# Kernel tuning notes

Measured on AMD Instinct MI355X. Metric: run time of the kernel, lower is better.

## Reference

```python
import jax, jax.numpy as jnp
import numpy as np

BLOCK_SIZE = 256

def setup_inputs() -> dict:
    key = jax.random.key(0)
    k1, k2, k3 = jax.random.split(key, 3)
    B, H, S, D = 2, 16, 2048, 128
    return {
        "query": jax.random.normal(k1, (B, H, S, D), dtype=jnp.float32),
        "key": jax.random.normal(k2, (B, H, S, D), dtype=jnp.float32),
        "value": jax.random.normal(k3, (B, H, S, D), dtype=jnp.float32),
    }

def reference(query, key, value):
    # Faithful translation of the (non-flash) blocked attention:
    # for each query block i and key block j, a FULL softmax is taken over
    # just that key block, and the per-block outputs are summed over j.
    B, H, S, D = query.shape
    bs = min(BLOCK_SIZE, S)
    nb = S // bs  # S chosen to be a multiple of block_size
    scale = D ** -0.5
    q = query.reshape(B, H, nb, bs, D)
    k = key.reshape(B, H, nb, bs, D)
    v = value.reshape(B, H, nb, bs, D)
    # scores: [B,H,nb_q,nb_k,bs_q,bs_k]
    scores = jnp.einsum('bhiqd,bhjkd->bhijqk', q, k) * scale
    # per key-block softmax (over last axis only, NOT global online softmax)
    w = jax.nn.softmax(scores, axis=-1)
    # weighted values, summed over key blocks j (matches output += block_output)
    out = jnp.einsum('bhijqk,bhjkd->bhiqd', w, v)
    return out.reshape(B, H, S, D)
```

## Files before the change

kernel.cpp:

```cpp
#include <hip/hip_runtime.h>
#include <stdint.h>

#define S_LEN 2048
#define D_DIM 128

typedef __attribute__((ext_vector_type(8)))  short bf16x8;
typedef __attribute__((ext_vector_type(4)))  short bf16x4;
typedef __attribute__((ext_vector_type(4)))  float f32x4;
typedef __attribute__((ext_vector_type(2)))  float f32x2;
typedef __attribute__((ext_vector_type(16))) float f32x16;

__device__ __forceinline__ short f2bf(float f) {
  union { float f; uint32_t u; } c; c.f = f;
  uint32_t u = c.u;
  u += 0x7fffu + ((u >> 16) & 1u);
  return (short)(u >> 16);
}
__device__ __forceinline__ uint32_t pk2bf(float a, float b) {
#if __has_builtin(__builtin_amdgcn_cvt_pk_bf16_f32)
  typedef __attribute__((ext_vector_type(2))) __bf16 bf2;
  union { bf2 v; uint32_t u; } cv;
  cv.v = __builtin_amdgcn_cvt_pk_bf16_f32(a, b);
  return cv.u;
#else
  return (uint32_t)(uint16_t)f2bf(a) | (((uint32_t)(uint16_t)f2bf(b)) << 16);
#endif
}
__device__ __forceinline__ float fexp2(float x) {
#if __has_builtin(__builtin_amdgcn_exp2f)
  return __builtin_amdgcn_exp2f(x);
#else
  return exp2f(x);
#endif
}
__device__ __forceinline__ bf16x8 mk8(uint32_t a, uint32_t b, uint32_t c, uint32_t d) {
  union { uint32_t u[4]; bf16x8 v; } x;
  x.u[0] = a; x.u[1] = b; x.u[2] = c; x.u[3] = d;
  return x.v;
}
__device__ __forceinline__ void gl_lds16(const short* g, short* l) {
  __builtin_amdgcn_global_load_lds((const __attribute__((address_space(1))) void*)g,
                                   (__attribute__((address_space(3))) void*)l, 16, 0, 0);
}

__global__ __launch_bounds__(256) void pre_kernel(
    const float* __restrict__ K, const float* __restrict__ V,
    short* __restrict__ Kb, short* __restrict__ Vt) {
  const int t = threadIdx.x;
  if (blockIdx.x >= 512) {
    int i0 = (blockIdx.x - 512) * 256 + t;
#pragma unroll
    for (int r = 0; r < 4; ++r) {
      int i = i0 + r * 524288;
      f32x4 v = ((const f32x4*)K)[i];
      *(uint2*)(Kb + (size_t)i * 4) = make_uint2(pk2bf(v[0], v[1]), pk2bf(v[2], v[3]));
    }
    return;
  }
  __shared__ __align__(16) uint32_t sU[128][64];
  const int vb = blockIdx.x;
  const int bh = vb >> 4;
  const int k0 = (vb & 15) * 128;
  const float* src = V + ((size_t)bh * S_LEN + k0) * D_DIM;
  {
    const int a = t & 31;
    const int E = 2 * (a & 15);
    const float* s0 = src + (size_t)(t >> 5) * 2 * D_DIM + a * 4;
#pragma unroll
    for (int p = 0; p < 8; ++p) {
      f32x4 vA = *(const f32x4*)(s0 + p * 16 * D_DIM);
      f32x4 vB = *(const f32x4*)(s0 + p * 16 * D_DIM + D_DIM);
      const int k2 = p * 8 + (t >> 5);
      const int col = k2 ^ E;
#pragma unroll
      for (int j = 0; j < 4; ++j)
        sU[4 * a + j][col] = pk2bf(vA[j], vB[j]);
    }
  }
  __syncthreads();
  {
    const int d = t >> 1;
    const int E = 2 * ((t >> 3) & 15);
    short* out = Vt + ((size_t)bh * D_DIM + d) * S_LEN + k0 + (t & 1) * 8;
#pragma unroll
    for (int g = 0; g < 8; ++g) {
      const int pb = g * 16 + (t & 1) * 8;
      const int kb1 = ((pb >> 4) << 4) + ((pb & 15) ? 4 : 0);
      const int k2a = kb1 >> 1;
      const int k2b = k2a + 4;
      uint2 lo = *(const uint2*)&sU[d][k2a ^ E];
      uint2 hi = *(const uint2*)&sU[d][k2b ^ E];
      uint4 o; o.x = lo.x; o.y = lo.y; o.z = hi.x; o.w = hi.y;
      *(uint4*)(out + g * 16) = o;
    }
  }
}

__global__ __launch_bounds__(256, 2) void attn_main(
    const short* __restrict__ Kb, const short* __restrict__ Vt,
    const float* __restrict__ Q, float* __restrict__ O) {
  __shared__ __align__(16) short ring[2][16384];
  __shared__ __align__(16) short sP[4096];
  __shared__ float sRed[128];
  __shared__ float sLinv[64];

  const int t = threadIdx.x;
  const int w = t >> 6;
  const int lane = t & 63;
  const int l31 = lane & 31;
  const int hi = lane >> 5;
  const int h = w & 1;
  const int qp = w >> 1;

  const int b = blockIdx.x;
  const int bh = (b & 7) * 4 + ((b >> 3) & 3);
  const int q0 = (b >> 5) * 64;

  const short* Kh = Kb + (size_t)bh * S_LEN * D_DIM;
  const short* Vh = Vt + (size_t)bh * D_DIM * S_LEN;

  const int kKey = t >> 4;
  const int kG   = (t & 15) ^ (kKey & 15);
  const int vD   = t >> 3;
  const int vG   = (t & 7) ^ (vD & 7);

  auto stageK = [&](int key0, int slot) {
    const short* src = Kh + (size_t)(key0 + kKey) * D_DIM + kG * 8;
    short* dst = &ring[slot][t * 8];
#pragma unroll
    for (int r = 0; r < 4; ++r) gl_lds16(src + r * 16 * D_DIM, dst + r * 2048);
  };
  auto stageV = [&](int key0, int slot) {
    const short* src = Vh + (size_t)vD * S_LEN + key0 + vG * 8;
    short* dst = &ring[slot][8192 + t * 8];
#pragma unroll
    for (int r = 0; r < 4; ++r) gl_lds16(src + (size_t)r * 32 * S_LEN, dst + r * 2048);
  };

  bf16x8 qf[8];
  {
    const float QSCALE = 0.12751743f;
    const float* Qg = Q + ((size_t)bh * S_LEN + q0 + qp * 32 + l31) * D_DIM;
#pragma unroll
    for (int ks = 0; ks < 8; ++ks) {
      f32x4 a = *(const f32x4*)(Qg + ks * 16 + hi * 8);
      f32x4 c = *(const f32x4*)(Qg + ks * 16 + hi * 8 + 4);
      qf[ks] = mk8(pk2bf(a[0] * QSCALE, a[1] * QSCALE), pk2bf(a[2] * QSCALE, a[3] * QSCALE),
                   pk2bf(c[0] * QSCALE, c[1] * QSCALE), pk2bf(c[2] * QSCALE, c[3] * QSCALE));
    }
  }

  int aK[8];
#pragma unroll
  for (int ks = 0; ks < 8; ++ks)
    aK[ks] = (h * 32 + l31) * 128 + (((2 * ks + hi) ^ (l31 & 15)) << 3);
  int aV[4];
#pragma unroll
  for (int u = 0; u < 4; ++u)
    aV[u] = (h * 64 + l31) * 64 + (((u * 2 + hi) ^ (l31 & 7)) << 3);

  f32x16 oa[2], oj[2], ojb[2];
#pragma unroll
  for (int d = 0; d < 2; ++d)
#pragma unroll
    for (int r = 0; r < 16; ++r) { oa[d][r] = 0.f; oj[d][r] = 0.f; ojb[d][r] = 0.f; }

  float ssum = 0.f;
  const int spOwn = ((qp * 2 + h) * 2) * 512 + lane * 8;

  stageK(0, 0); stageV(0, 0);

  for (int j = 0; j < 8; ++j) {
#pragma unroll
    for (int c = 0; c < 4; ++c) {
      const int G = j * 4 + c;
      const int slot = G & 1;
      __syncthreads();
      if (G + 1 < 32) { stageK((G + 1) * 64, slot ^ 1); stageV((G + 1) * 64, slot ^ 1); }

      if (c == 0 && j > 0) {
        f32x4 lv[4];
#pragma unroll
        for (int g = 0; g < 4; ++g) lv[g] = *(const f32x4*)&sLinv[qp * 32 + g * 8 + hi * 4];
#pragma unroll
        for (int d = 0; d < 2; ++d)
#pragma unroll
          for (int r = 0; r < 16; ++r) {
            oa[d][r] += (oj[d][r] + ojb[d][r]) * lv[r >> 2][r & 3];
            oj[d][r] = 0.f;
            ojb[d][r] = 0.f;
          }
      }

      const short* pK = &ring[slot][0];
      f32x16 sc0, sc1;
#pragma unroll
      for (int r = 0; r < 16; ++r) { sc0[r] = 0.f; sc1[r] = 0.f; }
#pragma unroll
      for (int ks = 0; ks < 4; ++ks) {
        bf16x8 a0 = *(const bf16x8*)(pK + aK[2 * ks]);
        bf16x8 a1 = *(const bf16x8*)(pK + aK[2 * ks + 1]);
        sc0 = __builtin_amdgcn_mfma_f32_32x32x16_bf16(a0, qf[2 * ks], sc0, 0, 0, 0);
        sc1 = __builtin_amdgcn_mfma_f32_32x32x16_bf16(a1, qf[2 * ks + 1], sc1, 0, 0, 0);
      }
      f32x16 sc;
#pragma unroll
      for (int r = 0; r < 16; ++r) sc[r] = fexp2(sc0[r] + sc1[r]);

      bf16x8 pf[2];
#pragma unroll
      for (int t2 = 0; t2 < 2; ++t2) {
        pf[t2] = mk8(pk2bf(sc[8 * t2 + 0], sc[8 * t2 + 1]), pk2bf(sc[8 * t2 + 2], sc[8 * t2 + 3]),
                     pk2bf(sc[8 * t2 + 4], sc[8 * t2 + 5]), pk2bf(sc[8 * t2 + 6], sc[8 * t2 + 7]));
        *(bf16x8*)(sP + spOwn + t2 * 512) = pf[t2];
      }
      {
        float a0 = sc[0] + sc[1], a1 = sc[2] + sc[3], a2 = sc[4] + sc[5], a3 = sc[6] + sc[7];
        float a4 = sc[8] + sc[9], a5 = sc[10] + sc[11], a6 = sc[12] + sc[13], a7 = sc[14] + sc[15];
        float b0 = a0 + a1, b1 = a2 + a3, b2 = a4 + a5, b3 = a6 + a7;
        ssum += (b0 + b1) + (b2 + b3);
      }
      if (c == 3) {
        ssum += __shfl_xor(ssum, 32);
        if (lane < 32) sRed[(qp * 32 + l31) * 2 + h] = ssum;
        ssum = 0.f;
      }
      __syncthreads();
      if (c == 3 && h == 0 && lane < 32) {
        f32x2 s2 = *(const f32x2*)&sRed[(qp * 32 + l31) * 2];
        sLinv[qp * 32 + l31] = __fdividef(1.0f, s2[0] + s2[1]);
      }

      const short* pV = &ring[slot][8192];
#pragma unroll
      for (int hw = 0; hw < 2; ++hw)
#pragma unroll
        for (int t2 = 0; t2 < 2; ++t2) {
          bf16x8 a = (hw == h) ? pf[t2]
                               : *(const bf16x8*)(sP + ((qp * 2 + hw) * 2 + t2) * 512 + lane * 8);
#pragma unroll
          for (int dt = 0; dt < 2; ++dt) {
            bf16x8 bv = *(const bf16x8*)(pV + aV[hw * 2 + t2] + dt * 2048);
            if (hw == 0)
              oj[dt] = __builtin_amdgcn_mfma_f32_32x32x16_bf16(a, bv, oj[dt], 0, 0, 0);
            else
              ojb[dt] = __builtin_amdgcn_mfma_f32_32x32x16_bf16(a, bv, ojb[dt], 0, 0, 0);
          }
        }
    }
  }

  __syncthreads();
  {
    f32x4 lv[4];
#pragma unroll
    for (int g = 0; g < 4; ++g) lv[g] = *(const f32x4*)&sLinv[qp * 32 + g * 8 + hi * 4];
    float* Og = O + ((size_t)bh * S_LEN + q0) * D_DIM;
#pragma unroll
    for (int d = 0; d < 2; ++d)
#pragma unroll
      for (int r = 0; r < 16; ++r) {
        float val = oa[d][r] + (oj[d][r] + ojb[d][r]) * lv[r >> 2][r & 3];
        int row = qp * 32 + (r & 3) + 8 * (r >> 2) + 4 * hi;
        int col = h * 64 + d * 32 + l31;
        Og[row * D_DIM + col] = val;
      }
  }
}

extern "C" void kernel_launch(void* const* d_in, const int* in_sizes, int n_in,
                              void* d_out, int out_size, void* d_ws, size_t ws_size,
                              hipStream_t stream) {
  const float* Q = (const float*)d_in[0];
  const float* K = (const float*)d_in[1];
  const float* V = (const float*)d_in[2];
  float* Out = (float*)d_out;
  const size_t tElems = (size_t)32 * S_LEN * D_DIM;

  short* Kb  = (short*)d_ws;
  short* Vtb = Kb + tElems;

  pre_kernel<<<2560, 256, 0, stream>>>(K, V, Kb, Vtb);
  attn_main<<<1024, 256, 0, stream>>>(Kb, Vtb, Q, Out);
}
```

Before: 222.9 us.

## Pre-swizzle V into MFMA fragment layout and load V directly to registers

The V transpose pre-pass now writes V in a fragment-major layout so each lane can load its MFMA B operands straight from global memory into registers, with no LDS staging. The V half of the LDS ring is removed, which halves the ring and LDS footprint and may allow more resident blocks. The per-row reciprocal sum is computed on the fly from sRed instead of through a separate sLinv pass, and the second block barrier becomes a raw waitcnt plus s_barrier. In exchange, V global-load latency now sits directly in each iteration, prefetched only at the start of the same step rather than a step ahead, and every wave re-reads V from global/L2.

```diff
diff --git a/kernel.cpp b/kernel.cpp
--- a/kernel.cpp
+++ b/kernel.cpp
@@ -81,7 +81,8 @@
   {
     const int d = t >> 1;
     const int E = 2 * ((t >> 3) & 15);
-    short* out = Vt + ((size_t)bh * D_DIM + d) * S_LEN + k0 + (t & 1) * 8;
+    short* outB = Vt + (size_t)bh * 262144 + d * 8;
+    const int g0 = k0 >> 3;
 #pragma unroll
     for (int g = 0; g < 8; ++g) {
       const int pb = g * 16 + (t & 1) * 8;
@@ -89,9 +90,9 @@
       const int k2a = kb1 >> 1;
       const int k2b = k2a + 4;
       uint2 lo = *(const uint2*)&sU[d][k2a ^ E];
-      uint2 hi = *(const uint2*)&sU[d][k2b ^ E];
-      uint4 o; o.x = lo.x; o.y = lo.y; o.z = hi.x; o.w = hi.y;
-      *(uint4*)(out + g * 16) = o;
+      uint2 hi2 = *(const uint2*)&sU[d][k2b ^ E];
+      uint4 o; o.x = lo.x; o.y = lo.y; o.z = hi2.x; o.w = hi2.y;
+      *(uint4*)(outB + (size_t)(g0 + (pb >> 3)) * 1024) = o;
     }
   }
 }
@@ -99,10 +100,9 @@
 __global__ __launch_bounds__(256, 2) void attn_main(
     const short* __restrict__ Kb, const short* __restrict__ Vt,
     const float* __restrict__ Q, float* __restrict__ O) {
-  __shared__ __align__(16) short ring[2][16384];
+  __shared__ __align__(16) short ring[2][8192];
   __shared__ __align__(16) short sP[4096];
   __shared__ float sRed[128];
-  __shared__ float sLinv[64];
 
   const int t = threadIdx.x;
   const int w = t >> 6;
@@ -117,12 +117,10 @@
   const int q0 = (b >> 5) * 64;
 
   const short* Kh = Kb + (size_t)bh * S_LEN * D_DIM;
-  const short* Vh = Vt + (size_t)bh * D_DIM * S_LEN;
+  const short* Vh2 = Vt + (size_t)bh * 262144;
 
   const int kKey = t >> 4;
   const int kG   = (t & 15) ^ (kKey & 15);
-  const int vD   = t >> 3;
-  const int vG   = (t & 7) ^ (vD & 7);
 
   auto stageK = [&](int key0, int slot) {
     const short* src = Kh + (size_t)(key0 + kKey) * D_DIM + kG * 8;
@@ -130,12 +128,8 @@
 #pragma unroll
     for (int r = 0; r < 4; ++r) gl_lds16(src + r * 16 * D_DIM, dst + r * 2048);
   };
-  auto stageV = [&](int key0, int slot) {
-    const short* src = Vh + (size_t)vD * S_LEN + key0 + vG * 8;
-    short* dst = &ring[slot][8192 + t * 8];
-#pragma unroll
-    for (int r = 0; r < 4; ++r) gl_lds16(src + (size_t)r * 32 * S_LEN, dst + r * 2048);
-  };
+
+  const short* Vbase = Vh2 + hi * 1024 + (h * 64 + l31) * 8;
 
   bf16x8 qf[8];
   {
@@ -154,10 +148,6 @@
 #pragma unroll
   for (int ks = 0; ks < 8; ++ks)
     aK[ks] = (h * 32 + l31) * 128 + (((2 * ks + hi) ^ (l31 & 15)) << 3);
-  int aV[4];
-#pragma unroll
-  for (int u = 0; u < 4; ++u)
-    aV[u] = (h * 64 + l31) * 64 + (((u * 2 + hi) ^ (l31 & 7)) << 3);
 
   f32x16 oa[2], oj[2], ojb[2];
 #pragma unroll
@@ -168,7 +158,19 @@
   float ssum = 0.f;
   const int spOwn = ((qp * 2 + h) * 2) * 512 + lane * 8;
 
-  stageK(0, 0); stageV(0, 0);
+  auto loadLv = [&](f32x4* lv) {
+#pragma unroll
+    for (int g = 0; g < 4; ++g) {
+      f32x4 p0 = *(const f32x4*)&sRed[(qp * 32 + g * 8 + 4 * hi) * 2];
+      f32x4 p1 = *(const f32x4*)&sRed[(qp * 32 + g * 8 + 4 * hi) * 2 + 4];
+      lv[g][0] = __fdividef(1.0f, p0[0] + p0[1]);
+      lv[g][1] = __fdividef(1.0f, p0[2] + p0[3]);
+      lv[g][2] = __fdividef(1.0f, p1[0] + p1[1]);
+      lv[g][3] = __fdividef(1.0f, p1[2] + p1[3]);
+    }
+  };
+
+  stageK(0, 0);
 
   for (int j = 0; j < 8; ++j) {
 #pragma unroll
@@ -176,12 +178,19 @@
       const int G = j * 4 + c;
       const int slot = G & 1;
       __syncthreads();
-      if (G + 1 < 32) { stageK((G + 1) * 64, slot ^ 1); stageV((G + 1) * 64, slot ^ 1); }
+
+      bf16x8 vf[8];
+#pragma unroll
+      for (int u = 0; u < 4; ++u)
+#pragma unroll
+        for (int dt = 0; dt < 2; ++dt)
+          vf[u * 2 + dt] = *(const bf16x8*)(Vbase + (size_t)G * 8192 + u * 2048 + dt * 256);
+
+      if (G + 1 < 32) stageK((G + 1) * 64, slot ^ 1);
 
       if (c == 0 && j > 0) {
         f32x4 lv[4];
-#pragma unroll
-        for (int g = 0; g < 4; ++g) lv[g] = *(const f32x4*)&sLinv[qp * 32 + g * 8 + hi * 4];
+        loadLv(lv);
 #pragma unroll
         for (int d = 0; d < 2; ++d)
 #pragma unroll
@@ -225,13 +234,9 @@
         if (lane < 32) sRed[(qp * 32 + l31) * 2 + h] = ssum;
         ssum = 0.f;
       }
-      __syncthreads();
-      if (c == 3 && h == 0 && lane < 32) {
-        f32x2 s2 = *(const f32x2*)&sRed[(qp * 32 + l31) * 2];
-        sLinv[qp * 32 + l31] = __fdividef(1.0f, s2[0] + s2[1]);
-      }
-
-      const short* pV = &ring[slot][8192];
+
+      asm volatile("s_waitcnt lgkmcnt(0)\n\ts_barrier" ::: "memory");
+
 #pragma unroll
       for (int hw = 0; hw < 2; ++hw)
 #pragma unroll
@@ -240,7 +245,7 @@
                                : *(const bf16x8*)(sP + ((qp * 2 + hw) * 2 + t2) * 512 + lane * 8);
 #pragma unroll
           for (int dt = 0; dt < 2; ++dt) {
-            bf16x8 bv = *(const bf16x8*)(pV + aV[hw * 2 + t2] + dt * 2048);
+            bf16x8 bv = vf[(hw * 2 + t2) * 2 + dt];
             if (hw == 0)
               oj[dt] = __builtin_amdgcn_mfma_f32_32x32x16_bf16(a, bv, oj[dt], 0, 0, 0);
             else
@@ -253,8 +258,7 @@
   __syncthreads();
   {
     f32x4 lv[4];
-#pragma unroll
-    for (int g = 0; g < 4; ++g) lv[g] = *(const f32x4*)&sLinv[qp * 32 + g * 8 + hi * 4];
+    loadLv(lv);
     float* Og = O + ((size_t)bh * S_LEN + q0) * D_DIM;
 #pragma unroll
     for (int d = 0; d < 2; ++d)
```

Result: slower. 263.5 us (+18.2%).

## Recompute full key-tile scores per wave to drop P exchange and mid-iteration barrier

Applied to the files above, without the earlier changes.

Each wave pair previously split the 64 keys of a tile, exchanged bf16 probabilities through shared memory and needed a second __syncthreads per tile plus a reciprocal stage. Now each wave computes QK^T for all 64 keys redundantly (splitting D for the PV product instead), keeping P in registers, removing the sP buffer and the extra barrier, and computing reciprocals at use. This doubles the QK MFMA and exp work per wave in exchange for fewer barriers and LDS traffic. The sRed write at c==3 and its later read rely on the next iteration's top barrier for ordering.

```diff
diff --git a/kernel.cpp b/kernel.cpp
--- a/kernel.cpp
+++ b/kernel.cpp
@@ -100,16 +100,14 @@
     const short* __restrict__ Kb, const short* __restrict__ Vt,
     const float* __restrict__ Q, float* __restrict__ O) {
   __shared__ __align__(16) short ring[2][16384];
-  __shared__ __align__(16) short sP[4096];
-  __shared__ float sRed[128];
-  __shared__ float sLinv[64];
+  __shared__ float sRed[64];
 
   const int t = threadIdx.x;
   const int w = t >> 6;
   const int lane = t & 63;
   const int l31 = lane & 31;
   const int hi = lane >> 5;
-  const int h = w & 1;
+  const int dh = w & 1;
   const int qp = w >> 1;
 
   const int b = blockIdx.x;
@@ -153,11 +151,11 @@
   int aK[8];
 #pragma unroll
   for (int ks = 0; ks < 8; ++ks)
-    aK[ks] = (h * 32 + l31) * 128 + (((2 * ks + hi) ^ (l31 & 15)) << 3);
+    aK[ks] = l31 * 128 + (((2 * ks + hi) ^ (l31 & 15)) << 3);
   int aV[4];
 #pragma unroll
   for (int u = 0; u < 4; ++u)
-    aV[u] = (h * 64 + l31) * 64 + (((u * 2 + hi) ^ (l31 & 7)) << 3);
+    aV[u] = (dh * 64 + l31) * 64 + (((u * 2 + hi) ^ (l31 & 7)) << 3);
 
   f32x16 oa[2], oj[2], ojb[2];
 #pragma unroll
@@ -166,7 +164,17 @@
     for (int r = 0; r < 16; ++r) { oa[d][r] = 0.f; oj[d][r] = 0.f; ojb[d][r] = 0.f; }
 
   float ssum = 0.f;
-  const int spOwn = ((qp * 2 + h) * 2) * 512 + lane * 8;
+
+  auto loadLv = [&](f32x4* lv) {
+#pragma unroll
+    for (int g = 0; g < 4; ++g) {
+      f32x4 s = *(const f32x4*)&sRed[qp * 32 + g * 8 + 4 * hi];
+      lv[g][0] = __fdividef(1.0f, s[0]);
+      lv[g][1] = __fdividef(1.0f, s[1]);
+      lv[g][2] = __fdividef(1.0f, s[2]);
+      lv[g][3] = __fdividef(1.0f, s[3]);
+    }
+  };
 
   stageK(0, 0); stageV(0, 0);
 
@@ -180,8 +188,7 @@
 
       if (c == 0 && j > 0) {
         f32x4 lv[4];
-#pragma unroll
-        for (int g = 0; g < 4; ++g) lv[g] = *(const f32x4*)&sLinv[qp * 32 + g * 8 + hi * 4];
+        loadLv(lv);
 #pragma unroll
         for (int d = 0; d < 2; ++d)
 #pragma unroll
@@ -197,64 +204,58 @@
 #pragma unroll
       for (int r = 0; r < 16; ++r) { sc0[r] = 0.f; sc1[r] = 0.f; }
 #pragma unroll
-      for (int ks = 0; ks < 4; ++ks) {
-        bf16x8 a0 = *(const bf16x8*)(pK + aK[2 * ks]);
-        bf16x8 a1 = *(const bf16x8*)(pK + aK[2 * ks + 1]);
-        sc0 = __builtin_amdgcn_mfma_f32_32x32x16_bf16(a0, qf[2 * ks], sc0, 0, 0, 0);
-        sc1 = __builtin_amdgcn_mfma_f32_32x32x16_bf16(a1, qf[2 * ks + 1], sc1, 0, 0, 0);
-      }
-      f32x16 sc;
-#pragma unroll
-      for (int r = 0; r < 16; ++r) sc[r] = fexp2(sc0[r] + sc1[r]);
-
-      bf16x8 pf[2];
+      for (int ks = 0; ks < 8; ++ks) {
+        bf16x8 a0 = *(const bf16x8*)(pK + aK[ks]);
+        bf16x8 a1 = *(const bf16x8*)(pK + aK[ks] + 4096);
+        sc0 = __builtin_amdgcn_mfma_f32_32x32x16_bf16(a0, qf[ks], sc0, 0, 0, 0);
+        sc1 = __builtin_amdgcn_mfma_f32_32x32x16_bf16(a1, qf[ks], sc1, 0, 0, 0);
+      }
+#pragma unroll
+      for (int r = 0; r < 16; ++r) { sc0[r] = fexp2(sc0[r]); sc1[r] = fexp2(sc1[r]); }
+
+      bf16x8 pf[4];
 #pragma unroll
       for (int t2 = 0; t2 < 2; ++t2) {
-        pf[t2] = mk8(pk2bf(sc[8 * t2 + 0], sc[8 * t2 + 1]), pk2bf(sc[8 * t2 + 2], sc[8 * t2 + 3]),
-                     pk2bf(sc[8 * t2 + 4], sc[8 * t2 + 5]), pk2bf(sc[8 * t2 + 6], sc[8 * t2 + 7]));
-        *(bf16x8*)(sP + spOwn + t2 * 512) = pf[t2];
+        pf[t2] = mk8(pk2bf(sc0[8 * t2 + 0], sc0[8 * t2 + 1]), pk2bf(sc0[8 * t2 + 2], sc0[8 * t2 + 3]),
+                     pk2bf(sc0[8 * t2 + 4], sc0[8 * t2 + 5]), pk2bf(sc0[8 * t2 + 6], sc0[8 * t2 + 7]));
+        pf[2 + t2] = mk8(pk2bf(sc1[8 * t2 + 0], sc1[8 * t2 + 1]), pk2bf(sc1[8 * t2 + 2], sc1[8 * t2 + 3]),
+                         pk2bf(sc1[8 * t2 + 4], sc1[8 * t2 + 5]), pk2bf(sc1[8 * t2 + 6], sc1[8 * t2 + 7]));
       }
       {
-        float a0 = sc[0] + sc[1], a1 = sc[2] + sc[3], a2 = sc[4] + sc[5], a3 = sc[6] + sc[7];
-        float a4 = sc[8] + sc[9], a5 = sc[10] + sc[11], a6 = sc[12] + sc[13], a7 = sc[14] + sc[15];
-        float b0 = a0 + a1, b1 = a2 + a3, b2 = a4 + a5, b3 = a6 + a7;
-        ssum += (b0 + b1) + (b2 + b3);
+        float a0 = sc0[0] + sc0[1], a1 = sc0[2] + sc0[3], a2 = sc0[4] + sc0[5], a3 = sc0[6] + sc0[7];
+        float a4 = sc0[8] + sc0[9], a5 = sc0[10] + sc0[11], a6 = sc0[12] + sc0[13], a7 = sc0[14] + sc0[15];
+        float b0 = sc1[0] + sc1[1], b1 = sc1[2] + sc1[3], b2 = sc1[4] + sc1[5], b3 = sc1[6] + sc1[7];
+        float b4 = sc1[8] + sc1[9], b5 = sc1[10] + sc1[11], b6 = sc1[12] + sc1[13], b7 = sc1[14] + sc1[15];
+        float c0 = (a0 + a1) + (a2 + a3), c1 = (a4 + a5) + (a6 + a7);
+        float c2 = (b0 + b1) + (b2 + b3), c3 = (b4 + b5) + (b6 + b7);
+        ssum += (c0 + c1) + (c2 + c3);
       }
       if (c == 3) {
         ssum += __shfl_xor(ssum, 32);
-        if (lane < 32) sRed[(qp * 32 + l31) * 2 + h] = ssum;
+        if (dh == 0 && lane < 32) sRed[qp * 32 + l31] = ssum;
         ssum = 0.f;
       }
-      __syncthreads();
-      if (c == 3 && h == 0 && lane < 32) {
-        f32x2 s2 = *(const f32x2*)&sRed[(qp * 32 + l31) * 2];
-        sLinv[qp * 32 + l31] = __fdividef(1.0f, s2[0] + s2[1]);
-      }
 
       const short* pV = &ring[slot][8192];
 #pragma unroll
-      for (int hw = 0; hw < 2; ++hw)
-#pragma unroll
-        for (int t2 = 0; t2 < 2; ++t2) {
-          bf16x8 a = (hw == h) ? pf[t2]
-                               : *(const bf16x8*)(sP + ((qp * 2 + hw) * 2 + t2) * 512 + lane * 8);
-#pragma unroll
-          for (int dt = 0; dt < 2; ++dt) {
-            bf16x8 bv = *(const bf16x8*)(pV + aV[hw * 2 + t2] + dt * 2048);
-            if (hw == 0)
-              oj[dt] = __builtin_amdgcn_mfma_f32_32x32x16_bf16(a, bv, oj[dt], 0, 0, 0);
-            else
-              ojb[dt] = __builtin_amdgcn_mfma_f32_32x32x16_bf16(a, bv, ojb[dt], 0, 0, 0);
-          }
+      for (int u = 0; u < 4; ++u) {
+        bf16x8 a = pf[u];
+#pragma unroll
+        for (int dt = 0; dt < 2; ++dt) {
+          bf16x8 bv = *(const bf16x8*)(pV + aV[u] + dt * 2048);
+          if (u < 2)
+            oj[dt] = __builtin_amdgcn_mfma_f32_32x32x16_bf16(a, bv, oj[dt], 0, 0, 0);
+          else
+            ojb[dt] = __builtin_amdgcn_mfma_f32_32x32x16_bf16(a, bv, ojb[dt], 0, 0, 0);
         }
+      }
     }
   }
 
   __syncthreads();
   {
     f32x4 lv[4];
-#pragma unroll
-    for (int g = 0; g < 4; ++g) lv[g] = *(const f32x4*)&sLinv[qp * 32 + g * 8 + hi * 4];
+    loadLv(lv);
     float* Og = O + ((size_t)bh * S_LEN + q0) * D_DIM;
 #pragma unroll
     for (int d = 0; d < 2; ++d)
@@ -262,7 +263,7 @@
       for (int r = 0; r < 16; ++r) {
         float val = oa[d][r] + (oj[d][r] + ojb[d][r]) * lv[r >> 2][r & 3];
         int row = qp * 32 + (r & 3) + 8 * (r >> 2) + 4 * hi;
-        int col = h * 64 + d * 32 + l31;
+        int col = dh * 64 + d * 32 + l31;
         Og[row * D_DIM + col] = val;
       }
   }
```

New measurement: 312.6 us. +40.2%, slower.

## Software-pipeline PV matmul one chunk behind QK and drop the second barrier

Applied to the files above, without the earlier changes.

Restructures the main loop so that the P·V MFMAs for chunk G-1 run after the QK^T and exp of chunk G. This removes the mid-iteration __syncthreads that separated writing P to shared memory from reading the partner wave's P. V staging is shifted one chunk later, the per-row reciprocal is computed directly from sRed instead of a separate sLinv pass, and a drain step after the loop handles the last PV. The intent is one barrier per chunk instead of two and better overlap of exp/convert work with MFMA, at the cost of more live registers (two P buffers) and trickier slot and rescale timing.

```diff
diff --git a/kernel.cpp b/kernel.cpp
--- a/kernel.cpp
+++ b/kernel.cpp
@@ -102,7 +102,6 @@
   __shared__ __align__(16) short ring[2][16384];
   __shared__ __align__(16) short sP[4096];
   __shared__ float sRed[128];
-  __shared__ float sLinv[64];
 
   const int t = threadIdx.x;
   const int w = t >> 6;
@@ -167,21 +166,44 @@
 
   float ssum = 0.f;
   const int spOwn = ((qp * 2 + h) * 2) * 512 + lane * 8;
-
-  stageK(0, 0); stageV(0, 0);
+  const int spFor = ((qp * 2 + (1 - h)) * 2) * 512 + lane * 8;
+
+  auto loadLv = [&](f32x4* lv) {
+#pragma unroll
+    for (int g = 0; g < 4; ++g) {
+      f32x4 p0 = *(const f32x4*)&sRed[(qp * 32 + g * 8 + 4 * hi) * 2];
+      f32x4 p1 = *(const f32x4*)&sRed[(qp * 32 + g * 8 + 4 * hi) * 2 + 4];
+      lv[g][0] = __fdividef(1.0f, p0[0] + p0[1]);
+      lv[g][1] = __fdividef(1.0f, p0[2] + p0[3]);
+      lv[g][2] = __fdividef(1.0f, p1[0] + p1[1]);
+      lv[g][3] = __fdividef(1.0f, p1[2] + p1[3]);
+    }
+  };
+
+  bf16x8 pfA[2], pfB[2];
+
+  stageK(0, 0);
 
   for (int j = 0; j < 8; ++j) {
 #pragma unroll
     for (int c = 0; c < 4; ++c) {
       const int G = j * 4 + c;
-      const int slot = G & 1;
+      const int kslot = c & 1;
       __syncthreads();
-      if (G + 1 < 32) { stageK((G + 1) * 64, slot ^ 1); stageV((G + 1) * 64, slot ^ 1); }
-
-      if (c == 0 && j > 0) {
+
+      if (G + 1 < 32) stageK((G + 1) * 64, kslot ^ 1);
+      stageV(G * 64, kslot);
+
+      bf16x8 pfF0, pfF1;
+      if (j > 0 || c > 0) {
+        pfF0 = *(const bf16x8*)(sP + spFor);
+        pfF1 = *(const bf16x8*)(sP + spFor + 512);
+      }
+      asm volatile("s_waitcnt lgkmcnt(0)\n\ts_barrier" ::: "memory");
+
+      if (c == 1 && j > 0) {
         f32x4 lv[4];
-#pragma unroll
-        for (int g = 0; g < 4; ++g) lv[g] = *(const f32x4*)&sLinv[qp * 32 + g * 8 + hi * 4];
+        loadLv(lv);
 #pragma unroll
         for (int d = 0; d < 2; ++d)
 #pragma unroll
@@ -192,7 +214,7 @@
           }
       }
 
-      const short* pK = &ring[slot][0];
+      const short* pK = &ring[kslot][0];
       f32x16 sc0, sc1;
 #pragma unroll
       for (int r = 0; r < 16; ++r) { sc0[r] = 0.f; sc1[r] = 0.f; }
@@ -203,20 +225,22 @@
         sc0 = __builtin_amdgcn_mfma_f32_32x32x16_bf16(a0, qf[2 * ks], sc0, 0, 0, 0);
         sc1 = __builtin_amdgcn_mfma_f32_32x32x16_bf16(a1, qf[2 * ks + 1], sc1, 0, 0, 0);
       }
-      f32x16 sc;
-#pragma unroll
-      for (int r = 0; r < 16; ++r) sc[r] = fexp2(sc0[r] + sc1[r]);
-
-      bf16x8 pf[2];
-#pragma unroll
-      for (int t2 = 0; t2 < 2; ++t2) {
-        pf[t2] = mk8(pk2bf(sc[8 * t2 + 0], sc[8 * t2 + 1]), pk2bf(sc[8 * t2 + 2], sc[8 * t2 + 3]),
-                     pk2bf(sc[8 * t2 + 4], sc[8 * t2 + 5]), pk2bf(sc[8 * t2 + 6], sc[8 * t2 + 7]));
-        *(bf16x8*)(sP + spOwn + t2 * 512) = pf[t2];
-      }
+#pragma unroll
+      for (int r = 0; r < 16; ++r) sc0[r] = fexp2(sc0[r] + sc1[r]);
+
       {
-        float a0 = sc[0] + sc[1], a1 = sc[2] + sc[3], a2 = sc[4] + sc[5], a3 = sc[6] + sc[7];
-        float a4 = sc[8] + sc[9], a5 = sc[10] + sc[11], a6 = sc[12] + sc[13], a7 = sc[14] + sc[15];
+        bf16x8 c0 = mk8(pk2bf(sc0[0], sc0[1]), pk2bf(sc0[2], sc0[3]),
+                        pk2bf(sc0[4], sc0[5]), pk2bf(sc0[6], sc0[7]));
+        bf16x8 c1 = mk8(pk2bf(sc0[8], sc0[9]), pk2bf(sc0[10], sc0[11]),
+                        pk2bf(sc0[12], sc0[13]), pk2bf(sc0[14], sc0[15]));
+        if ((c & 1) == 0) { pfA[0] = c0; pfA[1] = c1; }
+        else             { pfB[0] = c0; pfB[1] = c1; }
+        *(bf16x8*)(sP + spOwn) = c0;
+        *(bf16x8*)(sP + spOwn + 512) = c1;
+      }
+      {
+        float a0 = sc0[0] + sc0[1], a1 = sc0[2] + sc0[3], a2 = sc0[4] + sc0[5], a3 = sc0[6] + sc0[7];
+        float a4 = sc0[8] + sc0[9], a5 = sc0[10] + sc0[11], a6 = sc0[12] + sc0[13], a7 = sc0[14] + sc0[15];
         float b0 = a0 + a1, b1 = a2 + a3, b2 = a4 + a5, b3 = a6 + a7;
         ssum += (b0 + b1) + (b2 + b3);
       }
@@ -225,36 +249,51 @@
         if (lane < 32) sRed[(qp * 32 + l31) * 2 + h] = ssum;
         ssum = 0.f;
       }
-      __syncthreads();
-      if (c == 3 && h == 0 && lane < 32) {
-        f32x2 s2 = *(const f32x2*)&sRed[(qp * 32 + l31) * 2];
-        sLinv[qp * 32 + l31] = __fdividef(1.0f, s2[0] + s2[1]);
-      }
-
-      const short* pV = &ring[slot][8192];
-#pragma unroll
-      for (int hw = 0; hw < 2; ++hw)
-#pragma unroll
-        for (int t2 = 0; t2 < 2; ++t2) {
-          bf16x8 a = (hw == h) ? pf[t2]
-                               : *(const bf16x8*)(sP + ((qp * 2 + hw) * 2 + t2) * 512 + lane * 8);
-#pragma unroll
-          for (int dt = 0; dt < 2; ++dt) {
-            bf16x8 bv = *(const bf16x8*)(pV + aV[hw * 2 + t2] + dt * 2048);
-            if (hw == 0)
-              oj[dt] = __builtin_amdgcn_mfma_f32_32x32x16_bf16(a, bv, oj[dt], 0, 0, 0);
-            else
-              ojb[dt] = __builtin_amdgcn_mfma_f32_32x32x16_bf16(a, bv, ojb[dt], 0, 0, 0);
+
+      if (j > 0 || c > 0) {
+        const short* pV = &ring[kslot ^ 1][8192];
+#pragma unroll
+        for (int hw = 0; hw < 2; ++hw)
+#pragma unroll
+          for (int t2 = 0; t2 < 2; ++t2) {
+            bf16x8 pp = ((c & 1) == 0) ? pfB[t2] : pfA[t2];
+            bf16x8 a = (hw == h) ? pp : (t2 == 0 ? pfF0 : pfF1);
+#pragma unroll
+            for (int dt = 0; dt < 2; ++dt) {
+              bf16x8 bv = *(const bf16x8*)(pV + aV[hw * 2 + t2] + dt * 2048);
+              if (hw == 0)
+                oj[dt] = __builtin_amdgcn_mfma_f32_32x32x16_bf16(a, bv, oj[dt], 0, 0, 0);
+              else
+                ojb[dt] = __builtin_amdgcn_mfma_f32_32x32x16_bf16(a, bv, ojb[dt], 0, 0, 0);
+            }
           }
+      }
+    }
+  }
+
+  __syncthreads();
+  {
+    bf16x8 pfF0 = *(const bf16x8*)(sP + spFor);
+    bf16x8 pfF1 = *(const bf16x8*)(sP + spFor + 512);
+    const short* pV = &ring[1][8192];
+#pragma unroll
+    for (int hw = 0; hw < 2; ++hw)
+#pragma unroll
+      for (int t2 = 0; t2 < 2; ++t2) {
+        bf16x8 a = (hw == h) ? pfB[t2] : (t2 == 0 ? pfF0 : pfF1);
+#pragma unroll
+        for (int dt = 0; dt < 2; ++dt) {
+          bf16x8 bv = *(const bf16x8*)(pV + aV[hw * 2 + t2] + dt * 2048);
+          if (hw == 0)
+            oj[dt] = __builtin_amdgcn_mfma_f32_32x32x16_bf16(a, bv, oj[dt], 0, 0, 0);
+          else
+            ojb[dt] = __builtin_amdgcn_mfma_f32_32x32x16_bf16(a, bv, ojb[dt], 0, 0, 0);
         }
-    }
-  }
-
-  __syncthreads();
+      }
+  }
   {
     f32x4 lv[4];
-#pragma unroll
-    for (int g = 0; g < 4; ++g) lv[g] = *(const f32x4*)&sLinv[qp * 32 + g * 8 + hi * 4];
+    loadLv(lv);
     float* Og = O + ((size_t)bh * S_LEN + q0) * D_DIM;
 #pragma unroll
     for (int d = 0; d < 2; ++d)
```

New measurement: 273.9 us. 1.23x slower.
